# Performance work log

Hardware: AMD Instinct MI355X
Metric: run time of the kernel (lower is better)

The kernel has to match this reference:

```python
import jax, jax.numpy as jnp
import numpy as np

C = 256  # in_channels
B, N = 8, 2048


def setup_inputs() -> dict:
    key = jax.random.key(0)
    ks = jax.random.split(key, 9)
    s = 1.0 / np.sqrt(C)  # conv1d default init scale (approx)
    return {
        "x": jax.random.normal(ks[0], (B, C, N), jnp.float32),
        "wq": jax.random.normal(ks[1], (C, C), jnp.float32) * s,
        "bq": jax.random.normal(ks[2], (C,), jnp.float32) * s,
        "wk": jax.random.normal(ks[3], (C, C), jnp.float32) * s,
        "bk": jax.random.normal(ks[4], (C,), jnp.float32) * s,
        "wv": jax.random.normal(ks[5], (C, C), jnp.float32) * s,
        "bv": jax.random.normal(ks[6], (C,), jnp.float32) * s,
        "wo": jax.random.normal(ks[7], (C, C), jnp.float32) * s,
        "bo": jax.random.normal(ks[8], (C,), jnp.float32) * s,
    }


def reference(x, wq, bq, wk, bk, wv, bv, wo, bo):
    # 1x1 Conv1d == channel-wise linear: [C_out,C_in] x [B,C_in,N] -> [B,C_out,N]
    proj = lambda w, b, t: jnp.einsum('ci,bin->bcn', w, t) + b[None, :, None]
    q = proj(wq, bq, x)
    k = proj(wk, bk, x)
    v = proj(wv, bv, x)
    norm = 1.0 / (x.shape[1] ** 0.5)
    # scores: w[b,n,m] = sum_c q[b,c,n] k[b,c,m]
    w = jnp.einsum('bcn,bcm->bnm', q, k) * norm
    w = jax.nn.softmax(w, axis=2)
    # attn output: sum_m v[b,c,m] w[b,n,m] -> [B,C,N]
    av = jnp.einsum('bcm,bnm->bcn', v, w)
    out = proj(wo, bo, av)
    return x + out
```

## Files before the change

kernel.cpp:

```cpp
#include <hip/hip_runtime.h>
#include <hip/hip_bf16.h>

#define CCH 256
#define NSEQ 2048
#define BATCH 8

typedef __hip_bfloat16 bf16;
typedef short s8v __attribute__((ext_vector_type(8)));
typedef float f4v __attribute__((ext_vector_type(4)));
typedef float f16v __attribute__((ext_vector_type(16)));

struct __align__(8) bf16x4 { bf16 v[4]; };

__device__ __forceinline__ float b2f(bf16 h) { return __bfloat162float(h); }
__device__ __forceinline__ bf16 f2b(float f) { return __float2bfloat16(f); }

#define MFMA16(a, b, c) __builtin_amdgcn_mfma_f32_16x16x32_bf16((a), (b), (c), 0, 0, 0)
#define MFMA32(a, b, c) __builtin_amdgcn_mfma_f32_32x32x16_bf16((a), (b), (c), 0, 0, 0)

__device__ __forceinline__ void gload_lds16(const bf16* g, bf16* l) {
    __builtin_amdgcn_global_load_lds(
        (const __attribute__((address_space(1))) unsigned int*)(g),
        (__attribute__((address_space(3))) unsigned int*)(l), 16, 0, 0);
}

__global__ __launch_bounds__(256) void prepw_kernel(
    const float* __restrict__ wq, const float* __restrict__ wk,
    const float* __restrict__ wv,
    bf16* __restrict__ wqb, bf16* __restrict__ wkb, bf16* __restrict__ wvb)
{
    int base = (blockIdx.x * 256 + threadIdx.x) * 8;
    int mat = base >> 16, off = base & 65535;
    const float* s = (mat == 0) ? wq : (mat == 1) ? wk : wv;
    bf16* d       = (mat == 0) ? wqb : (mat == 1) ? wkb : wvb;
    #pragma unroll
    for (int j = 0; j < 8; ++j) d[off + j] = f2b(s[off + j]);
}

__global__ __launch_bounds__(256, 2) void qkvprep_kernel(
    const float* __restrict__ x,
    const bf16* __restrict__ Wq, const bf16* __restrict__ Wk,
    const bf16* __restrict__ Wv,
    const float* __restrict__ bq, const float* __restrict__ bk,
    const float* __restrict__ bv,
    bf16* __restrict__ qTt, bf16* __restrict__ kTt, bf16* __restrict__ Vt)
{
    __shared__ bf16 xs[64][260];

    const int tile = blockIdx.x;
    const int flat0 = tile * 64;
    const int phase = blockIdx.y;
    const int b = flat0 >> 11, nn = flat0 & 2047;
    const int tid = threadIdx.x;
    const int w = tid >> 6, lane = tid & 63;
    const int l15 = lane & 15, quad = lane >> 4;
    const float* xb = x + (size_t)b * CCH * NSEQ;

    #pragma unroll
    for (int i = 0; i < 16; ++i) {
        int f4i = i * 256 + tid;
        int c = f4i >> 4, nq = f4i & 15;
        float4 v4 = *(const float4*)&xb[(size_t)c * NSEQ + nn + nq * 4];
        xs[nq * 4 + 0][c] = f2b(v4.x);
        xs[nq * 4 + 1][c] = f2b(v4.y);
        xs[nq * 4 + 2][c] = f2b(v4.z);
        xs[nq * 4 + 3][c] = f2b(v4.w);
    }
    __syncthreads();

    s8v xf[8];
    #pragma unroll
    for (int t = 0; t < 8; ++t)
        xf[t] = *(const s8v*)&xs[w * 16 + l15][t * 32 + quad * 8];

    bf16* qt = qTt + (size_t)tile * 16384;
    bf16* kt = kTt + (size_t)tile * 16384;

    if (phase == 0) {
        #pragma unroll 2
        for (int cs = 0; cs < 16; ++cs) {
            const s8v* wr = (const s8v*)(Wq + (size_t)(cs * 16 + l15) * CCH);
            f4v a = {};
            #pragma unroll
            for (int t = 0; t < 8; ++t) a = MFMA16(xf[t], wr[t * 4 + quad], a);
            int c = cs * 16 + l15;
            float bb = bq[c];
            #pragma unroll
            for (int r = 0; r < 4; ++r) {
                int nl = w * 16 + quad * 4 + r;
                qt[(c >> 3) * 512 + nl * 8 + (c & 7)] = f2b((a[r] + bb) * 0.0625f);
            }
        }
        #pragma unroll 2
        for (int cs = 0; cs < 8; ++cs) {
            const s8v* wr = (const s8v*)(Wk + (size_t)(cs * 16 + l15) * CCH);
            f4v a = {};
            #pragma unroll
            for (int t = 0; t < 8; ++t) a = MFMA16(xf[t], wr[t * 4 + quad], a);
            int c = cs * 16 + l15;
            float bb = bk[c];
            #pragma unroll
            for (int r = 0; r < 4; ++r) {
                int nl = w * 16 + quad * 4 + r;
                kt[(c >> 3) * 512 + nl * 8 + (c & 7)] = f2b(a[r] + bb);
            }
        }
    } else {
        bf16* Vtb = Vt + (size_t)b * CCH * NSEQ;
        const int nb = nn + w * 16 + l15;
        const size_t vbase = (size_t)(nb >> 5) * 8192 + (nb & 31);
        #pragma unroll 2
        for (int cs = 0; cs < 16; ++cs) {
            const s8v* wr = (const s8v*)(Wv + (size_t)(cs * 16 + l15) * CCH);
            f4v a = {};
            #pragma unroll
            for (int t = 0; t < 8; ++t) a = MFMA16(wr[t * 4 + quad], xf[t], a);
            #pragma unroll
            for (int r = 0; r < 4; ++r) {
                int c = cs * 16 + quad * 4 + r;
                Vtb[vbase + (size_t)c * 32] = f2b(a[r] + bv[c]);
            }
        }
        #pragma unroll 2
        for (int cs = 8; cs < 16; ++cs) {
            const s8v* wr = (const s8v*)(Wk + (size_t)(cs * 16 + l15) * CCH);
            f4v a = {};
            #pragma unroll
            for (int t = 0; t < 8; ++t) a = MFMA16(xf[t], wr[t * 4 + quad], a);
            int c = cs * 16 + l15;
            float bb = bk[c];
            #pragma unroll
            for (int r = 0; r < 4; ++r) {
                int nl = w * 16 + quad * 4 + r;
                kt[(c >> 3) * 512 + nl * 8 + (c & 7)] = f2b(a[r] + bb);
            }
        }
    }
}

__global__ __launch_bounds__(256, 2) void flash_kernel(
    const bf16* __restrict__ qTt, const bf16* __restrict__ kTt,
    const bf16* __restrict__ Vt, bf16* __restrict__ Opart,
    float* __restrict__ lpart)
{
    __shared__ bf16 Kc[16384];
    __shared__ bf16 Ps[64][68];
    __shared__ float l_s[2][64];

    const int b = blockIdx.x, nt = blockIdx.y, ms = blockIdx.z;
    const int tid = threadIdx.x;
    const int W = tid >> 6, lane = tid & 63;
    const int l31 = lane & 31, h = lane >> 5;
    const int ng = W >> 1, mg = W & 1;
    const int mb = ms * 16;
    const bf16* Vtb = Vt + (size_t)b * CCH * NSEQ;

    s8v qf[16];
    {
        const bf16* qt = qTt + (size_t)(b * 32 + nt) * 16384;
        #pragma unroll
        for (int t = 0; t < 16; ++t)
            qf[t] = *(const s8v*)&qt[(t * 2 + h) * 512 + (ng * 32 + l31) * 8];
    }
    const bf16* vrow[2];
    #pragma unroll
    for (int cr = 0; cr < 2; ++cr)
        vrow[cr] = Vtb + (size_t)(W * 64 + cr * 32 + l31) * 32 + h * 8;

    f16v O[2][2] = {};
    float lacc[16] = {};

    {
        const bf16* kt = kTt + (size_t)(b * 32 + mb) * 16384;
        #pragma unroll
        for (int i = 0; i < 8; ++i) {
            int ch = W * 8 + i;
            gload_lds16(kt + ch * 512 + lane * 8, &Kc[ch * 512]);
        }
    }
    __syncthreads();

    for (int mt = 0; mt < 16; ++mt) {
        f16v S0 = {}, S1 = {};
        #pragma unroll
        for (int t = 0; t < 8; ++t) {
            s8v kf0 = *(const s8v*)&Kc[(t * 2 + h) * 512 + (mg * 32 + l31) * 8];
            s8v kf1 = *(const s8v*)&Kc[((t + 8) * 2 + h) * 512 + (mg * 32 + l31) * 8];
            S0 = MFMA32(qf[t], kf0, S0);
            S1 = MFMA32(qf[t + 8], kf1, S1);
        }
        s8v vf[2][4];
        #pragma unroll
        for (int ks = 0; ks < 4; ++ks)
            #pragma unroll
            for (int cr = 0; cr < 2; ++cr)
                vf[cr][ks] = *(const s8v*)(vrow[cr]
                    + (size_t)((mb + mt) * 2 + (ks >> 1)) * 8192
                    + (ks & 1) * 16);
        #pragma unroll
        for (int reg = 0; reg < 16; ++reg) {
            float e = __expf(fminf(S0[reg] + S1[reg], 60.f));
            lacc[reg] += e;
            int row = (reg & 3) + 8 * (reg >> 2) + 4 * h;
            Ps[ng * 32 + row][mg * 32 + l31] = f2b(e);
        }
        __syncthreads();

        if (mt < 15) {
            const bf16* kt = kTt + (size_t)(b * 32 + mb + mt + 1) * 16384;
            #pragma unroll
            for (int i = 0; i < 8; ++i) {
                int ch = W * 8 + i;
                gload_lds16(kt + ch * 512 + lane * 8, &Kc[ch * 512]);
            }
        }
        #pragma unroll
        for (int ks = 0; ks < 4; ++ks) {
            s8v pf0 = *(const s8v*)&Ps[l31][ks * 16 + h * 8];
            s8v pf1 = *(const s8v*)&Ps[32 + l31][ks * 16 + h * 8];
            O[0][0] = MFMA32(vf[0][ks], pf0, O[0][0]);
            O[0][1] = MFMA32(vf[0][ks], pf1, O[0][1]);
            O[1][0] = MFMA32(vf[1][ks], pf0, O[1][0]);
            O[1][1] = MFMA32(vf[1][ks], pf1, O[1][1]);
        }
        __syncthreads();
    }

    #pragma unroll
    for (int reg = 0; reg < 16; ++reg) {
        float s = lacc[reg];
        #pragma unroll
        for (int off = 1; off < 32; off <<= 1) s += __shfl_xor(s, off);
        lacc[reg] = s;
    }
    if (l31 == 0) {
        #pragma unroll
        for (int reg = 0; reg < 16; ++reg) {
            int row = (reg & 3) + 8 * (reg >> 2) + 4 * h;
            l_s[mg][ng * 32 + row] = lacc[reg];
        }
    }
    __syncthreads();
    const size_t pb = (size_t)(b * 32 + nt) * 2 + ms;
    if (tid < 64) lpart[pb * 64 + tid] = l_s[0][tid] + l_s[1][tid];

    bf16* Ob = Opart + pb * 16384;
    #pragma unroll
    for (int cr = 0; cr < 2; ++cr)
        #pragma unroll
        for (int g2 = 0; g2 < 2; ++g2) {
            int n = g2 * 32 + l31;
            #pragma unroll
            for (int q2 = 0; q2 < 4; ++q2) {
                bf16x4 pk;
                #pragma unroll
                for (int j = 0; j < 4; ++j) pk.v[j] = f2b(O[cr][g2][q2 * 4 + j]);
                int c = W * 64 + cr * 32 + q2 * 8 + 4 * h;
                *(bf16x4*)&Ob[(size_t)n * 256 + c] = pk;
            }
        }
}

__global__ __launch_bounds__(256, 2) void outproj_kernel(
    const bf16* __restrict__ Opart, const float* __restrict__ lpart,
    const float* __restrict__ Wo, const float* __restrict__ bo,
    const float* __restrict__ x, float* __restrict__ out)
{
    __shared__ bf16 avs[64][260];
    __shared__ float ils[64];

    const int bx = blockIdx.x;
    const int flat0 = bx * 64;
    const int c0 = blockIdx.y * 128;
    const int tid = threadIdx.x;
    const int w = tid >> 6, lane = tid & 63;
    const int l15 = lane & 15, quad = lane >> 4;

    if (tid < 64)
        ils[tid] = 1.f / (lpart[(size_t)(bx * 2) * 64 + tid]
                        + lpart[(size_t)(bx * 2 + 1) * 64 + tid]);
    __syncthreads();

    const bf16x4* O0 = (const bf16x4*)(Opart + (size_t)(bx * 2) * 16384);
    const bf16x4* O1 = O0 + 4096;
    #pragma unroll
    for (int i = 0; i < 16; ++i) {
        int u = i * 256 + tid;
        int n = u >> 6;
        bf16x4 a = O0[u], bb = O1[u];
        float il = ils[n];
        bf16x4 o;
        #pragma unroll
        for (int t = 0; t < 4; ++t)
            o.v[t] = f2b((b2f(a.v[t]) + b2f(bb.v[t])) * il);
        *(bf16x4*)&avs[n][(u & 63) * 4] = o;
    }
    __syncthreads();

    const int bidx = flat0 >> 11, nn = flat0 & 2047;
    const size_t base = (size_t)bidx * CCH * NSEQ;

    for (int g = 0; g < 2; ++g) {
        const int cg = c0 + g * 64 + w * 16;
        s8v af[8];
        #pragma unroll
        for (int t = 0; t < 8; ++t) {
            const float* wp = Wo + (size_t)(cg + l15) * CCH + t * 32 + quad * 8;
            float4 f0 = *(const float4*)wp;
            float4 f1 = *(const float4*)(wp + 4);
            bf16 a8[8] = { f2b(f0.x), f2b(f0.y), f2b(f0.z), f2b(f0.w),
                           f2b(f1.x), f2b(f1.y), f2b(f1.z), f2b(f1.w) };
            af[t] = *(const s8v*)a8;
        }
        f4v O[4] = {};
        #pragma unroll
        for (int nt = 0; nt < 4; ++nt)
            #pragma unroll
            for (int t = 0; t < 8; ++t) {
                s8v br = *(const s8v*)&avs[nt * 16 + l15][t * 32 + quad * 8];
                O[nt] = MFMA16(af[t], br, O[nt]);
            }
        #pragma unroll
        for (int r = 0; r < 4; ++r) {
            int c = cg + quad * 4 + r;
            float bb = bo[c];
            #pragma unroll
            for (int nt = 0; nt < 4; ++nt) {
                size_t idx = base + (size_t)c * NSEQ + nn + nt * 16 + l15;
                out[idx] = O[nt][r] + bb + x[idx];
            }
        }
    }
}

extern "C" void kernel_launch(void* const* d_in, const int* in_sizes, int n_in,
                              void* d_out, int out_size, void* d_ws, size_t ws_size,
                              hipStream_t stream) {
    (void)in_sizes; (void)n_in; (void)out_size; (void)ws_size;
    const float* x  = (const float*)d_in[0];
    const float* wq = (const float*)d_in[1];
    const float* bq = (const float*)d_in[2];
    const float* wk = (const float*)d_in[3];
    const float* bk = (const float*)d_in[4];
    const float* wv = (const float*)d_in[5];
    const float* bv = (const float*)d_in[6];
    const float* wo = (const float*)d_in[7];
    const float* bo = (const float*)d_in[8];
    float* out = (float*)d_out;

    const size_t T = (size_t)BATCH * CCH * NSEQ;
    bf16* qTt  = (bf16*)d_ws;
    bf16* kTt  = qTt + T;
    bf16* Vt   = kTt + T;
    bf16* wqb  = Vt + T;
    bf16* wkb  = wqb + 65536;
    bf16* wvb  = wkb + 65536;
    float* lpart = (float*)(wvb + 65536);
    bf16* Opart  = (bf16*)(lpart + 32768);

    prepw_kernel<<<96, 256, 0, stream>>>(wq, wk, wv, wqb, wkb, wvb);
    qkvprep_kernel<<<dim3(256, 2), 256, 0, stream>>>(
        x, wqb, wkb, wvb, bq, bk, bv, qTt, kTt, Vt);
    flash_kernel<<<dim3(8, 32, 2), 256, 0, stream>>>(qTt, kTt, Vt, Opart, lpart);
    outproj_kernel<<<dim3(256, 2), 256, 0, stream>>>(Opart, lpart, wo, bo, x, out);
}
```

Baseline: 188.9 us.

## Fold weight bf16 conversion into QKV projection and split work three ways

Drops the separate weight-conversion kernel: the QKV projection now reads fp32 weights directly and converts them to bf16 in registers. The grid's y dimension grows from 2 to 3 so each block computes exactly one of Q, K or V, which balances the per-block work, and launch bounds are raised to 3 blocks per SM. Each MFMA chain is split across two accumulators to shorten the dependency chain. The cost is that x is transposed and loaded three times instead of twice, and every block reads fp32 weights, doubling weight read bytes.

```diff
diff --git a/kernel.cpp b/kernel.cpp
--- a/kernel.cpp
+++ b/kernel.cpp
@@ -24,23 +24,18 @@
         (__attribute__((address_space(3))) unsigned int*)(l), 16, 0, 0);
 }
 
-__global__ __launch_bounds__(256) void prepw_kernel(
-    const float* __restrict__ wq, const float* __restrict__ wk,
-    const float* __restrict__ wv,
-    bf16* __restrict__ wqb, bf16* __restrict__ wkb, bf16* __restrict__ wvb)
-{
-    int base = (blockIdx.x * 256 + threadIdx.x) * 8;
-    int mat = base >> 16, off = base & 65535;
-    const float* s = (mat == 0) ? wq : (mat == 1) ? wk : wv;
-    bf16* d       = (mat == 0) ? wqb : (mat == 1) ? wkb : wvb;
-    #pragma unroll
-    for (int j = 0; j < 8; ++j) d[off + j] = f2b(s[off + j]);
-}
-
-__global__ __launch_bounds__(256, 2) void qkvprep_kernel(
+__device__ __forceinline__ s8v w8(const float* wp) {
+    float4 f0 = *(const float4*)wp;
+    float4 f1 = *(const float4*)(wp + 4);
+    bf16 a8[8] = { f2b(f0.x), f2b(f0.y), f2b(f0.z), f2b(f0.w),
+                   f2b(f1.x), f2b(f1.y), f2b(f1.z), f2b(f1.w) };
+    return *(const s8v*)a8;
+}
+
+__global__ __launch_bounds__(256, 3) void qkvprep_kernel(
     const float* __restrict__ x,
-    const bf16* __restrict__ Wq, const bf16* __restrict__ Wk,
-    const bf16* __restrict__ Wv,
+    const float* __restrict__ Wq, const float* __restrict__ Wk,
+    const float* __restrict__ Wv,
     const float* __restrict__ bq, const float* __restrict__ bk,
     const float* __restrict__ bv,
     bf16* __restrict__ qTt, bf16* __restrict__ kTt, bf16* __restrict__ Vt)
@@ -49,7 +44,7 @@
 
     const int tile = blockIdx.x;
     const int flat0 = tile * 64;
-    const int phase = blockIdx.y;
+    const int mat = blockIdx.y;
     const int b = flat0 >> 11, nn = flat0 & 2047;
     const int tid = threadIdx.x;
     const int w = tid >> 6, lane = tid & 63;
@@ -73,36 +68,29 @@
     for (int t = 0; t < 8; ++t)
         xf[t] = *(const s8v*)&xs[w * 16 + l15][t * 32 + quad * 8];
 
-    bf16* qt = qTt + (size_t)tile * 16384;
-    bf16* kt = kTt + (size_t)tile * 16384;
-
-    if (phase == 0) {
+    if (mat < 2) {
+        const float* Wm = mat ? Wk : Wq;
+        const float* bm = mat ? bk : bq;
+        bf16* ot = (mat ? kTt : qTt) + (size_t)tile * 16384;
+        const float scale = mat ? 1.0f : 0.0625f;
         #pragma unroll 2
         for (int cs = 0; cs < 16; ++cs) {
-            const s8v* wr = (const s8v*)(Wq + (size_t)(cs * 16 + l15) * CCH);
-            f4v a = {};
-            #pragma unroll
-            for (int t = 0; t < 8; ++t) a = MFMA16(xf[t], wr[t * 4 + quad], a);
+            const float* wrow = Wm + (size_t)(cs * 16 + l15) * CCH;
+            s8v wf[8];
+            #pragma unroll
+            for (int t = 0; t < 8; ++t) wf[t] = w8(wrow + t * 32 + quad * 8);
+            f4v a0 = {}, a1 = {};
+            #pragma unroll
+            for (int t = 0; t < 4; ++t) {
+                a0 = MFMA16(xf[t], wf[t], a0);
+                a1 = MFMA16(xf[t + 4], wf[t + 4], a1);
+            }
             int c = cs * 16 + l15;
-            float bb = bq[c];
+            float bb = bm[c];
             #pragma unroll
             for (int r = 0; r < 4; ++r) {
                 int nl = w * 16 + quad * 4 + r;
-                qt[(c >> 3) * 512 + nl * 8 + (c & 7)] = f2b((a[r] + bb) * 0.0625f);
-            }
-        }
-        #pragma unroll 2
-        for (int cs = 0; cs < 8; ++cs) {
-            const s8v* wr = (const s8v*)(Wk + (size_t)(cs * 16 + l15) * CCH);
-            f4v a = {};
-            #pragma unroll
-            for (int t = 0; t < 8; ++t) a = MFMA16(xf[t], wr[t * 4 + quad], a);
-            int c = cs * 16 + l15;
-            float bb = bk[c];
-            #pragma unroll
-            for (int r = 0; r < 4; ++r) {
-                int nl = w * 16 + quad * 4 + r;
-                kt[(c >> 3) * 512 + nl * 8 + (c & 7)] = f2b(a[r] + bb);
+                ot[(c >> 3) * 512 + nl * 8 + (c & 7)] = f2b((a0[r] + a1[r] + bb) * scale);
             }
         }
     } else {
@@ -111,28 +99,20 @@
         const size_t vbase = (size_t)(nb >> 5) * 8192 + (nb & 31);
         #pragma unroll 2
         for (int cs = 0; cs < 16; ++cs) {
-            const s8v* wr = (const s8v*)(Wv + (size_t)(cs * 16 + l15) * CCH);
-            f4v a = {};
-            #pragma unroll
-            for (int t = 0; t < 8; ++t) a = MFMA16(wr[t * 4 + quad], xf[t], a);
+            const float* wrow = Wv + (size_t)(cs * 16 + l15) * CCH;
+            s8v wf[8];
+            #pragma unroll
+            for (int t = 0; t < 8; ++t) wf[t] = w8(wrow + t * 32 + quad * 8);
+            f4v a0 = {}, a1 = {};
+            #pragma unroll
+            for (int t = 0; t < 4; ++t) {
+                a0 = MFMA16(wf[t], xf[t], a0);
+                a1 = MFMA16(wf[t + 4], xf[t + 4], a1);
+            }
             #pragma unroll
             for (int r = 0; r < 4; ++r) {
                 int c = cs * 16 + quad * 4 + r;
-                Vtb[vbase + (size_t)c * 32] = f2b(a[r] + bv[c]);
-            }
-        }
-        #pragma unroll 2
-        for (int cs = 8; cs < 16; ++cs) {
-            const s8v* wr = (const s8v*)(Wk + (size_t)(cs * 16 + l15) * CCH);
-            f4v a = {};
-            #pragma unroll
-            for (int t = 0; t < 8; ++t) a = MFMA16(xf[t], wr[t * 4 + quad], a);
-            int c = cs * 16 + l15;
-            float bb = bk[c];
-            #pragma unroll
-            for (int r = 0; r < 4; ++r) {
-                int nl = w * 16 + quad * 4 + r;
-                kt[(c >> 3) * 512 + nl * 8 + (c & 7)] = f2b(a[r] + bb);
+                Vtb[vbase + (size_t)c * 32] = f2b(a0[r] + a1[r] + bv[c]);
             }
         }
     }
@@ -304,14 +284,8 @@
         const int cg = c0 + g * 64 + w * 16;
         s8v af[8];
         #pragma unroll
-        for (int t = 0; t < 8; ++t) {
-            const float* wp = Wo + (size_t)(cg + l15) * CCH + t * 32 + quad * 8;
-            float4 f0 = *(const float4*)wp;
-            float4 f1 = *(const float4*)(wp + 4);
-            bf16 a8[8] = { f2b(f0.x), f2b(f0.y), f2b(f0.z), f2b(f0.w),
-                           f2b(f1.x), f2b(f1.y), f2b(f1.z), f2b(f1.w) };
-            af[t] = *(const s8v*)a8;
-        }
+        for (int t = 0; t < 8; ++t)
+            af[t] = w8(Wo + (size_t)(cg + l15) * CCH + t * 32 + quad * 8);
         f4v O[4] = {};
         #pragma unroll
         for (int nt = 0; nt < 4; ++nt)
@@ -352,15 +326,11 @@
     bf16* qTt  = (bf16*)d_ws;
     bf16* kTt  = qTt + T;
     bf16* Vt   = kTt + T;
-    bf16* wqb  = Vt + T;
-    bf16* wkb  = wqb + 65536;
-    bf16* wvb  = wkb + 65536;
-    float* lpart = (float*)(wvb + 65536);
+    float* lpart = (float*)(Vt + T);
     bf16* Opart  = (bf16*)(lpart + 32768);
 
-    prepw_kernel<<<96, 256, 0, stream>>>(wq, wk, wv, wqb, wkb, wvb);
-    qkvprep_kernel<<<dim3(256, 2), 256, 0, stream>>>(
-        x, wqb, wkb, wvb, bq, bk, bv, qTt, kTt, Vt);
+    qkvprep_kernel<<<dim3(256, 3), 256, 0, stream>>>(
+        x, wq, wk, wv, bq, bk, bv, qTt, kTt, Vt);
     flash_kernel<<<dim3(8, 32, 2), 256, 0, stream>>>(qTt, kTt, Vt, Opart, lpart);
     outproj_kernel<<<dim3(256, 2), 256, 0, stream>>>(Opart, lpart, wo, bo, x, out);
 }
```

Measured after the change: 244.0 us. 29.2% more time.
